# Performance work log

Measured on AMD Instinct MI355X. Metric: run time of the kernel, lower is better.

## Reference

```python
import jax, jax.numpy as jnp
import numpy as np

EPS_LN = 1e-6
STAB = 1e-3  # FAVOR+ relu-kernel numerical stabilizer

def layer_norm(x, gamma, beta):
    mu = jnp.mean(x, axis=-1, keepdims=True)
    var = jnp.mean(jnp.square(x - mu), axis=-1, keepdims=True)
    return (x - mu) * jax.lax.rsqrt(var + EPS_LN) * gamma + beta

def setup_inputs() -> dict:
    key = jax.random.key(0)
    B, L, E, H, F = 8, 2048, 1024, 16, 4096
    dh = E // H
    ks = jax.random.split(key, 12)
    s_attn = 1.0 / np.sqrt(E)
    s_ffn1 = 1.0 / np.sqrt(E)
    s_ffn2 = 1.0 / np.sqrt(F)
    return {
        "x": jax.random.normal(ks[0], (B, L, E), jnp.float32),
        "gamma1": jnp.ones((E,), jnp.float32),
        "beta1": jnp.zeros((E,), jnp.float32),
        "wq": jax.random.normal(ks[1], (E, H, dh), jnp.float32) * s_attn,
        "wk": jax.random.normal(ks[2], (E, H, dh), jnp.float32) * s_attn,
        "wv": jax.random.normal(ks[3], (E, H, dh), jnp.float32) * s_attn,
        "wo": jax.random.normal(ks[4], (H, dh, E), jnp.float32) * s_attn,
        "w1": jax.random.normal(ks[5], (E, F), jnp.float32) * s_ffn1,
        "b1": jnp.zeros((F,), jnp.float32),
        "w2": jax.random.normal(ks[6], (F, E), jnp.float32) * s_ffn2,
        "b2": jnp.zeros((E,), jnp.float32),
    }

def reference(x, gamma1, beta1, wq, wk, wv, wo, w1, b1, w2, b2):
    # ln_1 (layernorm1)
    ln1 = layer_norm(x, gamma1, beta1)
    # q/k/v head projections (bias-free DenseEinsum)
    q = jnp.einsum('ble,ehd->blhd', ln1, wq)
    k = jnp.einsum('ble,ehd->blhd', ln1, wk)
    v = jnp.einsum('ble,ehd->blhd', ln1, wv)
    # FAVOR+ relu kernel transformation (default, no projection matrix)
    qp = jax.nn.relu(q) + STAB  # [B,L,H,M]
    kp = jax.nn.relu(k) + STAB
    # non-causal linear attention: numerator and denominator
    kvs = jnp.einsum('blhm,blhd->bhmd', kp, v)          # [B,H,M,Dh]
    num = jnp.einsum('blhm,bhmd->blhd', qp, kvs)        # [B,L,H,Dh]
    ksum = jnp.sum(kp, axis=1)                          # [B,H,M]
    den = jnp.einsum('blhm,bhm->blh', qp, ksum)         # [B,L,H]
    att = num / den[..., None]
    attn_out = jnp.einsum('blhd,hde->ble', att, wo)
    add1 = attn_out + x
    # original code reuses layernorm1 here (layernorm2 unused)
    ln2 = layer_norm(add1, gamma1, beta1)
    h = jax.nn.gelu(jnp.einsum('ble,ef->blf', ln2, w1) + b1, approximate=False)
    out2 = jax.nn.gelu(jnp.einsum('blf,fe->ble', h, w2) + b2, approximate=False)
    # dropout is identity at inference
    return out2 + add1
```

## Files before the change

kernel.cpp:

```cpp
#include <hip/hip_runtime.h>
#include <hip/hip_bf16.h>
#include <math.h>

typedef float f32x4 __attribute__((ext_vector_type(4)));
typedef __bf16 bf16x8 __attribute__((ext_vector_type(8)));
typedef unsigned short u16x8 __attribute__((ext_vector_type(8)));
typedef unsigned short u16x4 __attribute__((ext_vector_type(4)));

__device__ __forceinline__ float bf2f(unsigned short u) {
    unsigned int x = ((unsigned int)u) << 16;
    float f; __builtin_memcpy(&f, &x, 4); return f;
}
__device__ __forceinline__ unsigned short f2bf(float f) {
    unsigned int x; __builtin_memcpy(&x, &f, 4);
    unsigned int r = x + 0x7fffu + ((x >> 16) & 1u);
    return (unsigned short)(r >> 16);
}
__device__ __forceinline__ float gelu_fast(float v) {
    float z2 = v * (1.5957691216f + 0.0713548162f * v * v);
    float e  = __expf(z2);
    float t  = 1.0f - 2.0f * __builtin_amdgcn_rcpf(1.0f + e);
    return 0.5f * v * (1.0f + t);
}
__device__ __forceinline__ void gload_lds16(const unsigned short* g, unsigned short* l) {
    __builtin_amdgcn_global_load_lds(
        (const __attribute__((address_space(1))) unsigned int*)g,
        (__attribute__((address_space(3))) unsigned int*)l, 16, 0, 0);
}

__global__ __launch_bounds__(256) void transpose_w(
    const float* __restrict__ in, unsigned short* __restrict__ out, int K, int N)
{
    __shared__ unsigned short tile[64][72];
    int nbn = N >> 6;
    int tk = (blockIdx.x / nbn) << 6;
    int tn = (blockIdx.x % nbn) << 6;
    int t = threadIdx.x;
    int r = t >> 2, c0 = (t & 3) * 16;
    #pragma unroll
    for (int i = 0; i < 16; i += 4) {
        float4 f = *(const float4*)(in + (size_t)(tk + r) * N + tn + c0 + i);
        tile[r][c0 + i + 0] = f2bf(f.x);
        tile[r][c0 + i + 1] = f2bf(f.y);
        tile[r][c0 + i + 2] = f2bf(f.z);
        tile[r][c0 + i + 3] = f2bf(f.w);
    }
    __syncthreads();
    u16x8 o0, o1;
    #pragma unroll
    for (int i = 0; i < 8; i++) { o0[i] = tile[c0 + i][r]; o1[i] = tile[c0 + 8 + i][r]; }
    *(u16x8*)(out + (size_t)(tn + r) * K + tk + c0)     = o0;
    *(u16x8*)(out + (size_t)(tn + r) * K + tk + c0 + 8) = o1;
}

__global__ __launch_bounds__(256) void transpose_bh(
    const unsigned short* __restrict__ in, unsigned short* __restrict__ out)
{
    int blk = blockIdx.x;
    int lt = blk & 31, h = (blk >> 5) & 15, b = blk >> 9;
    const unsigned short* src = in + ((size_t)(b * 2048 + lt * 64)) * 1024 + h * 64;
    unsigned short* dst = out + ((size_t)(b * 16 + h) * 64) * 2048 + lt * 64;
    __shared__ unsigned short tile[64][72];
    int t = threadIdx.x;
    int r = t >> 2, c0 = (t & 3) * 16;
    u16x8 v0 = *(const u16x8*)(src + (size_t)r * 1024 + c0);
    u16x8 v1 = *(const u16x8*)(src + (size_t)r * 1024 + c0 + 8);
    #pragma unroll
    for (int i = 0; i < 8; i++) { tile[r][c0 + i] = v0[i]; tile[r][c0 + 8 + i] = v1[i]; }
    __syncthreads();
    u16x8 o0, o1;
    #pragma unroll
    for (int i = 0; i < 8; i++) { o0[i] = tile[c0 + i][r]; o1[i] = tile[c0 + 8 + i][r]; }
    *(u16x8*)(dst + (size_t)r * 2048 + c0)     = o0;
    *(u16x8*)(dst + (size_t)r * 2048 + c0 + 8) = o1;
}

__global__ __launch_bounds__(256) void ksum_kernel(
    const unsigned short* __restrict__ kpT, float* __restrict__ ksum)
{
    int row = blockIdx.x * 4 + (threadIdx.x >> 6);
    int lane = threadIdx.x & 63;
    const unsigned short* src = kpT + (size_t)row * 2048;
    float s = 0.f;
    #pragma unroll
    for (int g = 0; g < 4; g++) {
        u16x8 v = *(const u16x8*)(src + g * 512 + lane * 8);
        #pragma unroll
        for (int q = 0; q < 8; q++) s += bf2f(v[q]);
    }
    #pragma unroll
    for (int o = 32; o > 0; o >>= 1) s += __shfl_down(s, o);
    if (lane == 0) ksum[row] = s;
}

__global__ __launch_bounds__(256) void kvs_mfma(
    const unsigned short* __restrict__ vT, const unsigned short* __restrict__ kpT,
    float* __restrict__ pbuf)
{
    int blk = blockIdx.x;
    int bh = blk >> 2, sp = blk & 3;
    const unsigned short* Abase = vT  + (size_t)bh * 64 * 2048 + sp * 512;
    const unsigned short* Bbase = kpT + (size_t)bh * 64 * 2048 + sp * 512;
    __shared__ unsigned short Al[64 * 64];
    __shared__ unsigned short Bl[64 * 64];
    int t = threadIdx.x;
    int lane = t & 63, wid = t >> 6;
    int l15 = lane & 15, l4 = lane >> 4;
    int wr = wid >> 1, wc = wid & 1;
    f32x4 acc[2][2] = {};
    for (int k0 = 0; k0 < 512; k0 += 64) {
        #pragma unroll
        for (int i = 0; i < 2; i++) {
            int chunk = i * 256 + t;
            int row = chunk >> 3, c = (chunk & 7) * 8;
            u16x8 av = *(const u16x8*)(Abase + (size_t)row * 2048 + k0 + c);
            u16x8 bv = *(const u16x8*)(Bbase + (size_t)row * 2048 + k0 + c);
            int off = (row * 128 + c * 2) ^ ((row & 7) << 4);
            *(u16x8*)((char*)Al + off) = av;
            *(u16x8*)((char*)Bl + off) = bv;
        }
        __syncthreads();
        #pragma unroll
        for (int kh = 0; kh < 2; kh++) {
            bf16x8 af[2], bf[2];
            #pragma unroll
            for (int mi = 0; mi < 2; mi++) {
                int row = wr * 32 + mi * 16 + l15;
                int off = (row * 128 + (kh * 32 + l4 * 8) * 2) ^ ((row & 7) << 4);
                af[mi] = *(const bf16x8*)((const char*)Al + off);
            }
            #pragma unroll
            for (int ni = 0; ni < 2; ni++) {
                int row = wc * 32 + ni * 16 + l15;
                int off = (row * 128 + (kh * 32 + l4 * 8) * 2) ^ ((row & 7) << 4);
                bf[ni] = *(const bf16x8*)((const char*)Bl + off);
            }
            #pragma unroll
            for (int mi = 0; mi < 2; mi++)
                #pragma unroll
                for (int ni = 0; ni < 2; ni++)
                    acc[mi][ni] = __builtin_amdgcn_mfma_f32_16x16x32_bf16(af[mi], bf[ni], acc[mi][ni], 0, 0, 0);
        }
        __syncthreads();
    }
    float* pb = pbuf + ((size_t)sp * 128 + bh) * 4096;
    #pragma unroll
    for (int mi = 0; mi < 2; mi++)
        #pragma unroll
        for (int ni = 0; ni < 2; ni++)
            #pragma unroll
            for (int j = 0; j < 4; j++) {
                int d = wr * 32 + mi * 16 + l4 * 4 + j;
                int m = wc * 32 + ni * 16 + l15;
                pb[d * 64 + m] = acc[mi][ni][j];
            }
}

__global__ __launch_bounds__(256) void reduce4(
    const float* __restrict__ pbuf, float* __restrict__ out)
{
    int i = blockIdx.x * 256 + threadIdx.x;
    float4 s = ((const float4*)pbuf)[i];
    #pragma unroll
    for (int sp = 1; sp < 4; sp++) {
        float4 p = ((const float4*)(pbuf + (size_t)sp * 524288))[i];
        s.x += p.x; s.y += p.y; s.z += p.z; s.w += p.w;
    }
    ((float4*)out)[i] = s;
}

__global__ __launch_bounds__(256) void ln_kernel(
    const float* __restrict__ x, const float* __restrict__ gamma,
    const float* __restrict__ beta, unsigned short* __restrict__ out)
{
    int row = blockIdx.x;
    int t = threadIdx.x;
    float4 v = ((const float4*)(x + (size_t)row * 1024))[t];
    float s  = v.x + v.y + v.z + v.w;
    float s2 = v.x * v.x + v.y * v.y + v.z * v.z + v.w * v.w;
    #pragma unroll
    for (int o = 32; o > 0; o >>= 1) { s += __shfl_down(s, o); s2 += __shfl_down(s2, o); }
    __shared__ float red[8];
    if ((t & 63) == 0) { red[t >> 6] = s; red[4 + (t >> 6)] = s2; }
    __syncthreads();
    s  = red[0] + red[1] + red[2] + red[3];
    s2 = red[4] + red[5] + red[6] + red[7];
    float mu  = s * (1.0f / 1024.0f);
    float var = s2 * (1.0f / 1024.0f) - mu * mu;
    float rs  = rsqrtf(var + 1e-6f);
    float4 g  = ((const float4*)gamma)[t];
    float4 be = ((const float4*)beta)[t];
    u16x4 o4;
    o4[0] = f2bf((v.x - mu) * rs * g.x + be.x);
    o4[1] = f2bf((v.y - mu) * rs * g.y + be.y);
    o4[2] = f2bf((v.z - mu) * rs * g.z + be.z);
    o4[3] = f2bf((v.w - mu) * rs * g.w + be.w);
    *(u16x4*)(out + (size_t)row * 1024 + t * 4) = o4;
}

template <int EP>
__global__ __launch_bounds__(512) void gemm256(
    const unsigned short* __restrict__ A, const unsigned short* __restrict__ Bt,
    void* __restrict__ C, const float* __restrict__ bias,
    const float* __restrict__ addv, int M, int N, int K)
{
    __shared__ unsigned short ldsbuf[69632];
    const int nbn = N >> 8;
    const int nwg = (M >> 8) * nbn;
    int bid = blockIdx.x;
    int wg = (bid & 7) * (nwg >> 3) + (bid >> 3);
    int tm = wg / nbn, tn = wg % nbn;
    const int tid = threadIdx.x;
    const int lane = tid & 63;
    const int l15 = lane & 15, l4 = lane >> 4;
    const int wid = tid >> 6;
    const int wr = wid >> 2, wc = wid & 3;

    const unsigned short* Ab = A + (size_t)(tm << 8) * K;
    const unsigned short* Bb = Bt + (size_t)(tn << 8) * K;

    const int swz   = (l15 & 7) << 4;
    const int koff0 = (l4 * 16) ^ swz;
    const int koff1 = (64 + l4 * 16) ^ swz;
    const int arow  = wr * 16384 + l15 * 128;
    const int brow  = wc * 8192  + l15 * 128;

    int goff[4];
    #pragma unroll
    for (int i = 0; i < 4; i++) {
        int cid = i * 512 + tid;
        int row = cid >> 3, c = cid & 7;
        goff[i] = row * K + ((c ^ (row & 7)) << 3);
    }
    const int ld0 = tid * 8;

    f32x4 acc[8][4] = {};
    const int NT = K >> 6;

#define STAGE_TILE(kt, slot)                                                   \
    {                                                                          \
        int k0_ = (kt) << 6;                                                   \
        _Pragma("unroll")                                                      \
        for (int i_ = 0; i_ < 4; i_++) {                                       \
            gload_lds16(Ab + (size_t)(goff[i_] + k0_), ldsbuf + (slot) * 32768 + ld0 + i_ * 4096); \
            gload_lds16(Bb + (size_t)(goff[i_] + k0_), ldsbuf + (slot) * 32768 + 16384 + ld0 + i_ * 4096); \
        }                                                                      \
    }

#define TILE_STEP(t_, s_)                                                      \
    {                                                                          \
        if ((t_) + 1 < NT) STAGE_TILE((t_) + 1, (s_) ^ 1);                     \
        const char* As_ = (const char*)(ldsbuf + (s_) * 32768);                \
        const char* Bs_ = (const char*)(ldsbuf + (s_) * 32768 + 16384);        \
        bf16x8 a_[8], b_[4];                                                   \
        _Pragma("unroll")                                                      \
        for (int m = 0; m < 8; m++) a_[m] = *(const bf16x8*)(As_ + arow + m * 2048 + koff0); \
        _Pragma("unroll")                                                      \
        for (int n = 0; n < 4; n++) b_[n] = *(const bf16x8*)(Bs_ + brow + n * 2048 + koff0); \
        __builtin_amdgcn_s_setprio(1);                                         \
        _Pragma("unroll")                                                      \
        for (int m = 0; m < 8; m++)                                            \
            _Pragma("unroll")                                                  \
            for (int n = 0; n < 4; n++)                                        \
                acc[m][n] = __builtin_amdgcn_mfma_f32_16x16x32_bf16(a_[m], b_[n], acc[m][n], 0, 0, 0); \
        __builtin_amdgcn_s_setprio(0);                                         \
        _Pragma("unroll")                                                      \
        for (int m = 0; m < 8; m++) a_[m] = *(const bf16x8*)(As_ + arow + m * 2048 + koff1); \
        _Pragma("unroll")                                                      \
        for (int n = 0; n < 4; n++) b_[n] = *(const bf16x8*)(Bs_ + brow + n * 2048 + koff1); \
        __builtin_amdgcn_s_setprio(1);                                         \
        _Pragma("unroll")                                                      \
        for (int m = 0; m < 8; m++)                                            \
            _Pragma("unroll")                                                  \
            for (int n = 0; n < 4; n++)                                        \
                acc[m][n] = __builtin_amdgcn_mfma_f32_16x16x32_bf16(a_[m], b_[n], acc[m][n], 0, 0, 0); \
        __builtin_amdgcn_s_setprio(0);                                         \
        asm volatile("s_waitcnt vmcnt(0)" ::: "memory");                       \
        __builtin_amdgcn_s_barrier();                                          \
    }

    STAGE_TILE(0, 0);
    asm volatile("s_waitcnt vmcnt(0)" ::: "memory");
    __builtin_amdgcn_s_barrier();

    for (int t = 0; t < NT; t += 2) {
        TILE_STEP(t, 0);
        TILE_STEP(t + 1, 1);
    }
#undef TILE_STEP
#undef STAGE_TILE

    int rbase = (tm << 8) + wr * 128;
    int cbase = (tn << 8) + wc * 64;
    if constexpr (EP == 2 || EP == 4) {
        #pragma unroll
        for (int n = 0; n < 4; n++) {
            int col = cbase + n * 16 + l15;
            float bval = 0.f;
            if constexpr (EP == 4) bval = bias[col];
            #pragma unroll
            for (int mf = 0; mf < 8; mf++) {
                #pragma unroll
                for (int j = 0; j < 4; j++) {
                    int row = rbase + mf * 16 + l4 * 4 + j;
                    float val = acc[mf][n][j];
                    if constexpr (EP == 4) val = gelu_fast(val + bval);
                    ((float*)C)[(size_t)row * N + col] = val + addv[(size_t)row * N + col];
                }
            }
        }
    } else {
        unsigned short* myl = ldsbuf + wid * 8704;
        #pragma unroll
        for (int n = 0; n < 4; n++) {
            int col = cbase + n * 16 + l15;
            float bval = 0.f;
            if constexpr (EP == 3) bval = bias[col];
            #pragma unroll
            for (int mf = 0; mf < 8; mf++) {
                #pragma unroll
                for (int j = 0; j < 4; j++) {
                    float val = acc[mf][n][j];
                    if constexpr (EP == 1) val = fmaxf(val, 0.f) + 1e-3f;
                    if constexpr (EP == 3) val = gelu_fast(val + bval);
                    myl[(mf * 16 + l4 * 4 + j) * 68 + n * 16 + l15] = f2bf(val);
                }
            }
        }
        #pragma unroll
        for (int c = 0; c < 16; c++) {
            int lrow = c * 8 + (lane >> 3);
            int cc = (lane & 7) * 8;
            u16x4 lo = *(const u16x4*)(myl + lrow * 68 + cc);
            u16x4 hi = *(const u16x4*)(myl + lrow * 68 + cc + 4);
            unsigned short* dst = (unsigned short*)C + (size_t)(rbase + lrow) * N + cbase + cc;
            *(u16x4*)dst = lo;
            *(u16x4*)(dst + 4) = hi;
        }
    }
}

__global__ __launch_bounds__(256) void att_num_kernel(
    const unsigned short* __restrict__ qp, const float* __restrict__ kvsT,
    const float* __restrict__ ksum, unsigned short* __restrict__ att)
{
    int blk = blockIdx.x;
    int t16 = blk & 15, h = (blk >> 4) & 15, b = blk >> 8;
    __shared__ unsigned short Al[128 * 64];
    __shared__ unsigned short Bl[64 * 64];
    __shared__ float kss[64];
    int tid = threadIdx.x;
    int lane = tid & 63, wid = tid >> 6;
    int l15 = lane & 15, l4 = lane >> 4;
    const unsigned short* Ab = qp + ((size_t)(b * 2048 + t16 * 128)) * 1024 + h * 64;
    const float* Bb  = kvsT + (size_t)(b * 16 + h) * 4096;
    const float* ksb = ksum + (b * 16 + h) * 64;
    #pragma unroll
    for (int i = 0; i < 4; i++) {
        int chunk = tid + i * 256;
        int row = chunk >> 3, c = (chunk & 7) * 8;
        u16x8 av = *(const u16x8*)(Ab + (size_t)row * 1024 + c);
        int off = (row * 128 + c * 2) ^ ((row & 7) << 4);
        *(u16x8*)((char*)Al + off) = av;
    }
    #pragma unroll
    for (int i = 0; i < 2; i++) {
        int chunk = tid + i * 256;
        int row = chunk >> 3, c = (chunk & 7) * 8;
        const float* src = Bb + (size_t)row * 64 + c;
        u16x8 bv;
        #pragma unroll
        for (int q = 0; q < 8; q++) bv[q] = f2bf(src[q]);
        int off = (row * 128 + c * 2) ^ ((row & 7) << 4);
        *(u16x8*)((char*)Bl + off) = bv;
    }
    if (tid < 64) kss[tid] = ksb[tid];
    __syncthreads();

    f32x4 acc[2][4] = {};
    #pragma unroll
    for (int kk = 0; kk < 64; kk += 32) {
        bf16x8 af[2], bfr[4];
        #pragma unroll
        for (int m = 0; m < 2; m++) {
            int row = wid * 32 + m * 16 + l15;
            int off = (row * 128 + (kk + l4 * 8) * 2) ^ ((row & 7) << 4);
            af[m] = *(const bf16x8*)((const char*)Al + off);
        }
        #pragma unroll
        for (int n = 0; n < 4; n++) {
            int row = n * 16 + l15;
            int off = (row * 128 + (kk + l4 * 8) * 2) ^ ((row & 7) << 4);
            bfr[n] = *(const bf16x8*)((const char*)Bl + off);
        }
        #pragma unroll
        for (int m = 0; m < 2; m++)
            #pragma unroll
            for (int n = 0; n < 4; n++)
                acc[m][n] = __builtin_amdgcn_mfma_f32_16x16x32_bf16(af[m], bfr[n], acc[m][n], 0, 0, 0);
    }
    __syncthreads();

    #pragma unroll
    for (int m = 0; m < 2; m++) {
        #pragma unroll
        for (int j = 0; j < 4; j++) {
            int lrow = wid * 32 + m * 16 + l4 * 4 + j;
            float den = 0.f;
            #pragma unroll
            for (int mm = 0; mm < 64; mm += 8) {
                int off = (lrow * 128 + mm * 2) ^ ((lrow & 7) << 4);
                u16x8 a8 = *(const u16x8*)((const char*)Al + off);
                #pragma unroll
                for (int q = 0; q < 8; q++) den += bf2f(a8[q]) * kss[mm + q];
            }
            float rden = 1.0f / den;
            size_t grow = (size_t)(b * 2048 + t16 * 128 + lrow);
            #pragma unroll
            for (int n = 0; n < 4; n++) {
                int col = h * 64 + n * 16 + l15;
                att[grow * 1024 + col] = f2bf(acc[m][n][j] * rden);
            }
        }
    }
}

extern "C" void kernel_launch(void* const* d_in, const int* in_sizes, int n_in,
                              void* d_out, int out_size, void* d_ws, size_t ws_size,
                              hipStream_t stream) {
    (void)in_sizes; (void)n_in; (void)out_size; (void)ws_size;
    const float* x      = (const float*)d_in[0];
    const float* gamma1 = (const float*)d_in[1];
    const float* beta1  = (const float*)d_in[2];
    const float* wq     = (const float*)d_in[3];
    const float* wk     = (const float*)d_in[4];
    const float* wv     = (const float*)d_in[5];
    const float* wo     = (const float*)d_in[6];
    const float* w1     = (const float*)d_in[7];
    const float* b1     = (const float*)d_in[8];
    const float* w2     = (const float*)d_in[9];
    const float* b2     = (const float*)d_in[10];
    float* out = (float*)d_out;

    const size_t MB = 1024 * 1024;
    char* ws = (char*)d_ws;
    unsigned short* wq_bt = (unsigned short*)(ws + 0 * MB);
    unsigned short* wk_bt = (unsigned short*)(ws + 2 * MB);
    unsigned short* wv_bt = (unsigned short*)(ws + 4 * MB);
    unsigned short* wo_bt = (unsigned short*)(ws + 6 * MB);
    unsigned short* w1_bt = (unsigned short*)(ws + 8 * MB);
    unsigned short* w2_bt = (unsigned short*)(ws + 16 * MB);
    unsigned short* lnbuf = (unsigned short*)(ws + 24 * MB);
    unsigned short* kpT   = (unsigned short*)(ws + 24 * MB);
    float*          add1  = (float*)(ws + 56 * MB);
    unsigned short* vT    = (unsigned short*)(ws + 56 * MB);
    float*          pbuf  = (float*)(ws + 88 * MB);
    unsigned short* qp    = (unsigned short*)(ws + 120 * MB);
    unsigned short* kp    = (unsigned short*)(ws + 152 * MB);
    unsigned short* vb    = (unsigned short*)(ws + 184 * MB);
    float*          kvsT  = (float*)(ws + 216 * MB);
    float*          ksum  = (float*)(ws + 218 * MB);
    unsigned short* hbuf  = (unsigned short*)(ws + 120 * MB);

    dim3 blk(256), blk512(512);
    transpose_w<<<dim3(256),  blk, 0, stream>>>(wq, wq_bt, 1024, 1024);
    transpose_w<<<dim3(256),  blk, 0, stream>>>(wk, wk_bt, 1024, 1024);
    transpose_w<<<dim3(256),  blk, 0, stream>>>(wv, wv_bt, 1024, 1024);
    transpose_w<<<dim3(256),  blk, 0, stream>>>(wo, wo_bt, 1024, 1024);
    transpose_w<<<dim3(1024), blk, 0, stream>>>(w1, w1_bt, 1024, 4096);
    transpose_w<<<dim3(1024), blk, 0, stream>>>(w2, w2_bt, 4096, 1024);
    ln_kernel<<<dim3(16384), blk, 0, stream>>>(x, gamma1, beta1, lnbuf);
    gemm256<1><<<dim3(256), blk512, 0, stream>>>(lnbuf, wq_bt, qp, nullptr, nullptr, 16384, 1024, 1024);
    gemm256<1><<<dim3(256), blk512, 0, stream>>>(lnbuf, wk_bt, kp, nullptr, nullptr, 16384, 1024, 1024);
    gemm256<0><<<dim3(256), blk512, 0, stream>>>(lnbuf, wv_bt, vb, nullptr, nullptr, 16384, 1024, 1024);
    transpose_bh<<<dim3(4096), blk, 0, stream>>>(kp, kpT);
    transpose_bh<<<dim3(4096), blk, 0, stream>>>(vb, vT);
    ksum_kernel<<<dim3(2048), blk, 0, stream>>>(kpT, ksum);
    kvs_mfma<<<dim3(512), blk, 0, stream>>>(vT, kpT, pbuf);
    reduce4<<<dim3(512), blk, 0, stream>>>(pbuf, kvsT);
    att_num_kernel<<<dim3(2048), blk, 0, stream>>>(qp, kvsT, ksum, qp);
    gemm256<2><<<dim3(256), blk512, 0, stream>>>(qp, wo_bt, add1, nullptr, x, 16384, 1024, 1024);
    ln_kernel<<<dim3(16384), blk, 0, stream>>>(add1, gamma1, beta1, lnbuf);
    gemm256<3><<<dim3(1024), blk512, 0, stream>>>(lnbuf, w1_bt, hbuf, b1, nullptr, 16384, 4096, 1024);
    gemm256<4><<<dim3(256),  blk512, 0, stream>>>(hbuf, w2_bt, out, b2, add1, 16384, 1024, 4096);
}
```

Baseline: 685.8 us.

## Switch GEMM to 4-stage K=32 pipeline with partial vmcnt waits

The bf16 GEMM main loop moves from a double-buffered K=64 tile to a four-slot ring of K=32 tiles, prefetching three tiles ahead. It waits on vmcnt(8) instead of vmcnt(0), so later loads stay in flight while the current tile computes. The XOR swizzle on the LDS layout is dropped for a plain row layout. This risks LDS bank conflicts on the fragment reads, adds a barrier per 32-wide K step, and issues redundant clamped prefetches of the last tile near the end.

```diff
diff --git a/kernel.cpp b/kernel.cpp
--- a/kernel.cpp
+++ b/kernel.cpp
@@ -219,44 +219,42 @@
     const unsigned short* Ab = A + (size_t)(tm << 8) * K;
     const unsigned short* Bb = Bt + (size_t)(tn << 8) * K;
 
-    const int swz   = (l15 & 7) << 4;
-    const int koff0 = (l4 * 16) ^ swz;
-    const int koff1 = (64 + l4 * 16) ^ swz;
-    const int arow  = wr * 16384 + l15 * 128;
-    const int brow  = wc * 8192  + l15 * 128;
-
-    int goff[4];
-    #pragma unroll
-    for (int i = 0; i < 4; i++) {
+    const int arow = wr * 8192 + l15 * 64 + l4 * 16;
+    const int brow = wc * 4096 + l15 * 64 + l4 * 16;
+
+    int goff[2];
+    #pragma unroll
+    for (int i = 0; i < 2; i++) {
         int cid = i * 512 + tid;
-        int row = cid >> 3, c = cid & 7;
-        goff[i] = row * K + ((c ^ (row & 7)) << 3);
+        goff[i] = (cid >> 2) * K + (cid & 3) * 8;
     }
     const int ld0 = tid * 8;
 
     f32x4 acc[8][4] = {};
-    const int NT = K >> 6;
-
-#define STAGE_TILE(kt, slot)                                                   \
+    const int NT = K >> 5;
+
+#define STAGE(kt, slot)                                                        \
     {                                                                          \
-        int k0_ = (kt) << 6;                                                   \
+        int k0_ = (kt) << 5;                                                   \
         _Pragma("unroll")                                                      \
-        for (int i_ = 0; i_ < 4; i_++) {                                       \
-            gload_lds16(Ab + (size_t)(goff[i_] + k0_), ldsbuf + (slot) * 32768 + ld0 + i_ * 4096); \
-            gload_lds16(Bb + (size_t)(goff[i_] + k0_), ldsbuf + (slot) * 32768 + 16384 + ld0 + i_ * 4096); \
+        for (int i_ = 0; i_ < 2; i_++) {                                       \
+            gload_lds16(Ab + (size_t)(goff[i_] + k0_), ldsbuf + (slot) * 16384 + ld0 + i_ * 4096); \
+            gload_lds16(Bb + (size_t)(goff[i_] + k0_), ldsbuf + (slot) * 16384 + 8192 + ld0 + i_ * 4096); \
         }                                                                      \
     }
 
 #define TILE_STEP(t_, s_)                                                      \
     {                                                                          \
-        if ((t_) + 1 < NT) STAGE_TILE((t_) + 1, (s_) ^ 1);                     \
-        const char* As_ = (const char*)(ldsbuf + (s_) * 32768);                \
-        const char* Bs_ = (const char*)(ldsbuf + (s_) * 32768 + 16384);        \
+        int pf_ = (t_) + 3;                                                    \
+        int pfk_ = pf_ < NT ? pf_ : NT - 1;    \
+        STAGE(pfk_, (s_ + 3) & 3);                                             \
+        const char* As_ = (const char*)(ldsbuf + (s_) * 16384);                \
+        const char* Bs_ = (const char*)(ldsbuf + (s_) * 16384 + 8192);         \
         bf16x8 a_[8], b_[4];                                                   \
         _Pragma("unroll")                                                      \
-        for (int m = 0; m < 8; m++) a_[m] = *(const bf16x8*)(As_ + arow + m * 2048 + koff0); \
+        for (int m = 0; m < 8; m++) a_[m] = *(const bf16x8*)(As_ + arow + m * 1024); \
         _Pragma("unroll")                                                      \
-        for (int n = 0; n < 4; n++) b_[n] = *(const bf16x8*)(Bs_ + brow + n * 2048 + koff0); \
+        for (int n = 0; n < 4; n++) b_[n] = *(const bf16x8*)(Bs_ + brow + n * 1024); \
         __builtin_amdgcn_s_setprio(1);                                         \
         _Pragma("unroll")                                                      \
         for (int m = 0; m < 8; m++)                                            \
@@ -264,31 +262,27 @@
             for (int n = 0; n < 4; n++)                                        \
                 acc[m][n] = __builtin_amdgcn_mfma_f32_16x16x32_bf16(a_[m], b_[n], acc[m][n], 0, 0, 0); \
         __builtin_amdgcn_s_setprio(0);                                         \
-        _Pragma("unroll")                                                      \
-        for (int m = 0; m < 8; m++) a_[m] = *(const bf16x8*)(As_ + arow + m * 2048 + koff1); \
-        _Pragma("unroll")                                                      \
-        for (int n = 0; n < 4; n++) b_[n] = *(const bf16x8*)(Bs_ + brow + n * 2048 + koff1); \
-        __builtin_amdgcn_s_setprio(1);                                         \
-        _Pragma("unroll")                                                      \
-        for (int m = 0; m < 8; m++)                                            \
-            _Pragma("unroll")                                                  \
-            for (int n = 0; n < 4; n++)                                        \
-                acc[m][n] = __builtin_amdgcn_mfma_f32_16x16x32_bf16(a_[m], b_[n], acc[m][n], 0, 0, 0); \
-        __builtin_amdgcn_s_setprio(0);                                         \
-        asm volatile("s_waitcnt vmcnt(0)" ::: "memory");                       \
+        asm volatile("s_waitcnt vmcnt(8)" ::: "memory");                       \
         __builtin_amdgcn_s_barrier();                                          \
     }
 
-    STAGE_TILE(0, 0);
+    STAGE(0, 0);
+    STAGE(1, 1);
+    STAGE(2, 2);
+    asm volatile("s_waitcnt vmcnt(8)" ::: "memory");
+    __builtin_amdgcn_s_barrier();
+
+    for (int t = 0; t < NT; t += 4) {
+        TILE_STEP(t, 0);
+        TILE_STEP(t + 1, 1);
+        TILE_STEP(t + 2, 2);
+        TILE_STEP(t + 3, 3);
+    }
+#undef TILE_STEP
+#undef STAGE
+
     asm volatile("s_waitcnt vmcnt(0)" ::: "memory");
     __builtin_amdgcn_s_barrier();
-
-    for (int t = 0; t < NT; t += 2) {
-        TILE_STEP(t, 0);
-        TILE_STEP(t + 1, 1);
-    }
-#undef TILE_STEP
-#undef STAGE_TILE
 
     int rbase = (tm << 8) + wr * 128;
     int cbase = (tn << 8) + wc * 64;
```

Result: slower. 714.4 us (+4.2%).
